# Performance work log

Hardware: AMD Instinct MI355X
Metric: run time of the kernel (lower is better)

The kernel has to match this reference:

```python
import jax, jax.numpy as jnp
import numpy as np

NEG = -1e9  # stand-in for -inf mask fill (avoids NaN, softmax weight ~0)
EPS = 1e-5  # torch LayerNorm default


def layer_norm(x, g, b):
    mu = jnp.mean(x, axis=-1, keepdims=True)
    var = jnp.mean(jnp.square(x - mu), axis=-1, keepdims=True)
    return (x - mu) * jax.lax.rsqrt(var + EPS) * g + b


def _forward(x, context, batch_lengths, max_len,
             Wq1, Wk1, Wv1, Wq2, Wk2, Wv2,
             ln1_g, ln1_b, ln2_g, ln2_b, ln3_g, ln3_b,
             fc1_w, fc1_b, fc2_w, fc2_b):
    B, L, E = x.shape
    H, _, dk = Wq1.shape
    pos = jnp.arange(L)
    valid = pos[None, :] < batch_lengths[:, None]                  # [B,L]
    out_mask = valid[:, :, None].astype(x.dtype)                   # [B,L,1] (outputMask)
    key_bias = jnp.where(valid, 0.0, NEG)[:, None, None, :]        # [B,1,1,L] (attnMask on keys)
    causal_bias = jnp.where(pos[:, None] >= pos[None, :], 0.0, NEG)  # [L,L] decoding mask
    scale = 1.0 / jnp.sqrt(jnp.asarray(dk, x.dtype))

    def mha(qk_src, v_src, Wq, Wk, Wv, causal):
        # Q,K from qk_src, V from v_src (faithful to Head.forward)
        m = out_mask[:, None]                                      # [B,1,L,1]
        Q = jnp.einsum('ble,hed->bhld', qk_src, Wq) * m
        K = jnp.einsum('ble,hed->bhld', qk_src, Wk) * m
        V = jnp.einsum('ble,hed->bhld', v_src, Wv) * m
        e = jnp.einsum('bhid,bhjd->bhij', Q, K) + key_bias
        if causal:
            e = e + causal_bias
        s = jax.nn.softmax(e * scale, axis=-1)
        o = jnp.einsum('bhij,bhjd->bhid', s, V)
        return o.transpose(0, 2, 1, 3).reshape(B, L, E)            # concat heads

    z = mha(x, x, Wq1, Wk1, Wv1, causal=True) * out_mask
    x1 = layer_norm(x + z, ln1_g, ln1_b)
    # cross block: Q,K from context, V from x1 (as in source)
    z = mha(context, x1, Wq2, Wk2, Wv2, causal=False) * out_mask
    x2 = layer_norm(x1 + z, ln2_g, ln2_b)
    h = jax.nn.relu(x2 @ fc1_w + fc1_b) * out_mask
    z = (h @ fc2_w + fc2_b) * out_mask
    return layer_norm(x2 + z, ln3_g, ln3_b)


def setup_inputs() -> dict:
    B, L, E, H = 8, 1024, 1024, 16
    dk = E // H
    key = jax.random.key(0)
    ks = jax.random.split(key, 16)
    w = lambda k, s: jax.random.normal(k, s, jnp.float32) * 0.02
    return {
        'x': jax.random.normal(ks[0], (B, L, E), jnp.float32),
        'context': jax.random.normal(ks[1], (B, L, E), jnp.float32),
        'batch_lengths': jax.random.randint(ks[2], (B,), 1, L + 1),
        'max_len': L,
        'Wq1': w(ks[3], (H, E, dk)), 'Wk1': w(ks[4], (H, E, dk)), 'Wv1': w(ks[5], (H, E, dk)),
        'Wq2': w(ks[6], (H, E, dk)), 'Wk2': w(ks[7], (H, E, dk)), 'Wv2': w(ks[8], (H, E, dk)),
        'ln1_g': jnp.ones((E,), jnp.float32), 'ln1_b': jnp.zeros((E,), jnp.float32),
        'ln2_g': jnp.ones((E,), jnp.float32), 'ln2_b': jnp.zeros((E,), jnp.float32),
        'ln3_g': jnp.ones((E,), jnp.float32), 'ln3_b': jnp.zeros((E,), jnp.float32),
        'fc1_w': w(ks[9], (E, E)), 'fc1_b': jnp.zeros((E,), jnp.float32),
        'fc2_w': w(ks[10], (E, E)), 'fc2_b': jnp.zeros((E,), jnp.float32),
    }


def reference(x, context, batch_lengths, max_len,
              Wq1, Wk1, Wv1, Wq2, Wk2, Wv2,
              ln1_g, ln1_b, ln2_g, ln2_b, ln3_g, ln3_b,
              fc1_w, fc1_b, fc2_w, fc2_b):
    return _forward(x, context, batch_lengths, max_len,
                    Wq1, Wk1, Wv1, Wq2, Wk2, Wv2,
                    ln1_g, ln1_b, ln2_g, ln2_b, ln3_g, ln3_b,
                    fc1_w, fc1_b, fc2_w, fc2_b)
```

## Files before the change

### kernel.cpp

```cpp
#include <hip/hip_runtime.h>


typedef unsigned short u16;
typedef unsigned int u32;
typedef __attribute__((ext_vector_type(8))) short bf16x8;
typedef __attribute__((ext_vector_type(4))) float f32x4;

#define Bv 8
#define Lv 1024
#define Ev 1024
#define Hv 16
#define DKv 64
#define Mv (Bv * Lv)

#if defined(__has_builtin)
# if __has_builtin(__builtin_amdgcn_global_load_lds)
#  define HAS_GLL 1
# endif
#endif
#ifndef HAS_GLL
# define HAS_GLL 0
#endif

#if HAS_GLL
__device__ __forceinline__ void gll16(const u16* g, u16* l) {
    __builtin_amdgcn_global_load_lds(
        (const __attribute__((address_space(1))) void*)(unsigned long long)(g),
        (__attribute__((address_space(3))) void*)(unsigned)(unsigned long long)(l),
        16, 0, 0);
}
#endif

__device__ __forceinline__ u16 f2bf(float f) {
    u32 u = __float_as_uint(f);
    u += 0x7fffu + ((u >> 16) & 1u);
    return (u16)(u >> 16);
}
__device__ __forceinline__ u32 pack2(float a, float b) {
    u32 ua = __float_as_uint(a); ua += 0x7fffu + ((ua >> 16) & 1u);
    u32 ub = __float_as_uint(b); ub += 0x7fffu + ((ub >> 16) & 1u);
    return (ua >> 16) | (ub & 0xffff0000u);
}
__device__ __forceinline__ float bf_lo(u32 u) { return __uint_as_float(u << 16); }
__device__ __forceinline__ float bf_hi(u32 u) { return __uint_as_float(u & 0xffff0000u); }

__global__ __launch_bounds__(256) void prep_k(
    const float* __restrict__ x, const float* __restrict__ ctx,
    const float* __restrict__ wq1, const float* __restrict__ wk1, const float* __restrict__ wv1,
    const float* __restrict__ wq2, const float* __restrict__ wk2, const float* __restrict__ wv2,
    const float* __restrict__ f1, const float* __restrict__ f2,
    u16* __restrict__ xb, u16* __restrict__ cb, u16* __restrict__ WT) {
    const int id = blockIdx.x, t = threadIdx.x;
    if (id < 16384) {
        const float* s = (id < 8192) ? x : ctx;
        u16* d = (id < 8192) ? xb : cb;
        const int i4 = ((id & 8191) * 256 + t) * 4;
        float4 v = *(const float4*)(s + i4);
        uint2 o = {pack2(v.x, v.y), pack2(v.z, v.w)};
        *(uint2*)(d + i4) = o;
        return;
    }
    __shared__ float tl[32][33];
    const int tx = t & 31, ty = t >> 5;
    if (id < 16384 + 6144) {
        const int wi = (id - 16384) >> 10;
        const int tile = (id - 16384) & 1023;
        const float* s = (wi == 0) ? wq1 : (wi == 1) ? wk1 : (wi == 2) ? wv1
                       : (wi == 3) ? wq2 : (wi == 4) ? wk2 : wv2;
        u16* d = WT + (size_t)wi * Ev * Ev;
        const int h = tile >> 6, rem = tile & 63;
        const int d0 = (rem & 1) * 32, e0 = (rem >> 1) * 32;
#pragma unroll
        for (int i = 0; i < 4; i++)
            tl[ty + i * 8][tx] = s[(size_t)h * Ev * DKv + (size_t)(e0 + ty + i * 8) * DKv + d0 + tx];
        __syncthreads();
#pragma unroll
        for (int i = 0; i < 4; i++)
            d[(size_t)(h * DKv + d0 + ty + i * 8) * Ev + e0 + tx] = f2bf(tl[tx][ty + i * 8]);
    } else {
        const int wi = (id - 16384 - 6144) >> 10;
        const int tile = (id - 16384 - 6144) & 1023;
        const float* s = wi ? f2 : f1;
        u16* d = WT + (size_t)(6 + wi) * Ev * Ev;
        const int n0 = (tile & 31) * 32, k0 = (tile >> 5) * 32;
#pragma unroll
        for (int i = 0; i < 4; i++)
            tl[ty + i * 8][tx] = s[(size_t)(k0 + ty + i * 8) * Ev + n0 + tx];
        __syncthreads();
#pragma unroll
        for (int i = 0; i < 4; i++)
            d[(size_t)(n0 + ty + i * 8) * Ev + k0 + tx] = f2bf(tl[tx][ty + i * 8]);
    }
}

template <int BIAS, int RELU, int TRANSW>
__global__ __launch_bounds__(256) void mgemm(const u16* __restrict__ A,
                                             const u16* __restrict__ Wt,
                                             const float* __restrict__ bias,
                                             u16* __restrict__ O0, u16* __restrict__ O1,
                                             u16* __restrict__ O2,
                                             const int* __restrict__ lens) {
    __shared__ u16 Alds[2][16 * 512];
    __shared__ u16 Blds[2][16 * 512];
    const int tid = threadIdx.x;
    const int w = tid >> 6, l = tid & 63;
    const int lc = l & 15, lq = l >> 4;
    const int row0 = blockIdx.y * 128, col0 = blockIdx.x * 128;
    const int which = col0 >> 10, colL = col0 & 1023;
    u16* C = (which == 0) ? O0 : (which == 1 ? O1 : O2);
    const bool tr = (TRANSW == which);

    int len = lens[row0 >> 10];
    len = min(max(len, 0), Lv);
    if ((row0 & (Lv - 1)) >= len) {
        const int rr = tid >> 1, cc = (tid & 1) * 64;
        u16* p = tr ? C + (size_t)(colL + rr) * Mv + row0 + cc
                    : C + (size_t)(row0 + rr) * Ev + colL + cc;
        uint4 z4 = {0u, 0u, 0u, 0u};
#pragma unroll
        for (int i = 0; i < 8; i++) *(uint4*)(p + i * 8) = z4;
        return;
    }

    const int wm4 = (w >> 1) * 4, wn4 = (w & 1) * 4;
    f32x4 acc[4][4];
#pragma unroll
    for (int i = 0; i < 4; i++)
#pragma unroll
        for (int j = 0; j < 4; j++) acc[i][j] = (f32x4){0.f, 0.f, 0.f, 0.f};

    const u16* Ag[4]; const u16* Bg[4];
    int lof[4];
#pragma unroll
    for (int i = 0; i < 4; i++) {
        const int g16 = 2 * w + (i >> 1), k32 = i & 1;
        Ag[i] = A  + (size_t)(row0 + g16 * 16 + lc) * Ev + k32 * 32 + lq * 8;
        Bg[i] = Wt + (size_t)(col0 + g16 * 16 + lc) * Ev + k32 * 32 + lq * 8;
        lof[i] = (g16 * 2 + k32) * 512;
    }

#if HAS_GLL
#pragma unroll
    for (int i = 0; i < 4; i++) { gll16(Ag[i], &Alds[0][lof[i]]); gll16(Bg[i], &Blds[0][lof[i]]); }
#pragma unroll
    for (int i = 0; i < 4; i++) { gll16(Ag[i] + 64, &Alds[1][lof[i]]); gll16(Bg[i] + 64, &Blds[1][lof[i]]); }

    for (int t = 0; t < 16; ++t) {
        const int p = t & 1;
        if (t < 15) asm volatile("s_waitcnt vmcnt(8)" ::: "memory");
        else        asm volatile("s_waitcnt vmcnt(0)" ::: "memory");
        __builtin_amdgcn_s_barrier();
        const u16* Ab = &Alds[p][0];
        const u16* Bb = &Blds[p][0];
#pragma unroll
        for (int km = 0; km < 2; km++) {
            bf16x8 af[4], bfr[4];
#pragma unroll
            for (int mt = 0; mt < 4; mt++)
                af[mt] = *(const bf16x8*)(Ab + ((wm4 + mt) * 2 + km) * 512 + l * 8);
#pragma unroll
            for (int nt = 0; nt < 4; nt++)
                bfr[nt] = *(const bf16x8*)(Bb + ((wn4 + nt) * 2 + km) * 512 + l * 8);
#pragma unroll
            for (int mt = 0; mt < 4; mt++)
#pragma unroll
                for (int nt = 0; nt < 4; nt++)
                    acc[mt][nt] = __builtin_amdgcn_mfma_f32_16x16x32_bf16(
                        af[mt], bfr[nt], acc[mt][nt], 0, 0, 0);
        }
        __builtin_amdgcn_s_barrier();
        if (t < 14) {
            const int koff = (t + 2) * 64;
#pragma unroll
            for (int i = 0; i < 4; i++) {
                gll16(Ag[i] + koff, &Alds[p][lof[i]]);
                gll16(Bg[i] + koff, &Blds[p][lof[i]]);
            }
        }
    }
#else
    for (int t = 0; t < 16; ++t) {
        const int koff = t * 64;
#pragma unroll
        for (int i = 0; i < 4; i++) {
            *(uint4*)(&Alds[0][lof[i] + l * 8]) = *(const uint4*)(Ag[i] + koff);
            *(uint4*)(&Blds[0][lof[i] + l * 8]) = *(const uint4*)(Bg[i] + koff);
        }
        __syncthreads();
#pragma unroll
        for (int km = 0; km < 2; km++) {
            bf16x8 af[4], bfr[4];
#pragma unroll
            for (int mt = 0; mt < 4; mt++)
                af[mt] = *(const bf16x8*)(&Alds[0][((wm4 + mt) * 2 + km) * 512 + l * 8]);
#pragma unroll
            for (int nt = 0; nt < 4; nt++)
                bfr[nt] = *(const bf16x8*)(&Blds[0][((wn4 + nt) * 2 + km) * 512 + l * 8]);
#pragma unroll
            for (int mt = 0; mt < 4; mt++)
#pragma unroll
                for (int nt = 0; nt < 4; nt++)
                    acc[mt][nt] = __builtin_amdgcn_mfma_f32_16x16x32_bf16(
                        af[mt], bfr[nt], acc[mt][nt], 0, 0, 0);
        }
        __syncthreads();
    }
#endif

    float bv[4];
#pragma unroll
    for (int nt = 0; nt < 4; nt++)
        bv[nt] = BIAS ? bias[colL + wn4 * 16 + nt * 16 + lc] : 0.f;

#pragma unroll
    for (int mt = 0; mt < 4; mt++) {
        const int rowb = row0 + wm4 * 16 + mt * 16 + lq * 4;
#pragma unroll
        for (int nt = 0; nt < 4; nt++) {
            const int col = colL + wn4 * 16 + nt * 16 + lc;
            float v[4];
#pragma unroll
            for (int r = 0; r < 4; r++) {
                float xv = acc[mt][nt][r] + bv[nt];
                if (RELU) xv = fmaxf(xv, 0.f);
                v[r] = (((rowb + r) & (Lv - 1)) >= len) ? 0.f : xv;
            }
            if (tr) {
                uint2 o = {pack2(v[0], v[1]), pack2(v[2], v[3])};
                *(uint2*)(C + (size_t)col * Mv + rowb) = o;
            } else {
#pragma unroll
                for (int r = 0; r < 4; r++)
                    C[(size_t)(rowb + r) * Ev + col] = f2bf(v[r]);
            }
        }
    }
}

template <int CAUSAL>
__global__ __launch_bounds__(256) void mattn(u16* __restrict__ QZ,
                                             const u16* __restrict__ K,
                                             const u16* __restrict__ VT,
                                             const int* __restrict__ lens) {
    __shared__ u16 Kt[2][16 * 512];
    __shared__ u16 Vt[2][16 * 512];
    __shared__ u16 Pt[4 * 4 * 512];
    const int b = blockIdx.z, h = blockIdx.y, qb = blockIdx.x;
    const int q0 = qb * 128;
    const int tid = threadIdx.x;
    const int w = tid >> 6, l = tid & 63;
    const int lc = l & 15, lq = l >> 4;
    int len = lens[b];
    len = min(max(len, 0), Lv);

    if (q0 >= len) {
        const int zr = tid >> 1, zc = (tid & 1) * 32;
        uint4 z4 = {0u, 0u, 0u, 0u};
        uint4* p = (uint4*)(QZ + (size_t)(b * Lv + q0 + zr) * Ev + h * DKv + zc);
        p[0] = z4; p[1] = z4; p[2] = z4; p[3] = z4;
        return;
    }

    bf16x8 qf[2][2];
#pragma unroll
    for (int mt = 0; mt < 2; mt++)
#pragma unroll
        for (int k2 = 0; k2 < 2; k2++)
            qf[mt][k2] = *(const bf16x8*)(QZ + (size_t)(b * Lv + q0 + w * 32 + mt * 16 + lc) * Ev +
                                          h * DKv + k2 * 32 + lq * 8);

    f32x4 of[2][4];
#pragma unroll
    for (int mt = 0; mt < 2; mt++)
#pragma unroll
        for (int nd = 0; nd < 4; nd++) of[mt][nd] = (f32x4){0.f, 0.f, 0.f, 0.f};
    float mrow[2][4], lrow[2][4];
#pragma unroll
    for (int mt = 0; mt < 2; mt++)
#pragma unroll
        for (int r = 0; r < 4; r++) { mrow[mt][r] = -1e30f; lrow[mt][r] = 0.f; }

    const u16* Kg[4]; const u16* Vg[4];
    int kof[4], vof[4];
#pragma unroll
    for (int i = 0; i < 4; i++) {
        const int k16 = 2 * w + (i >> 1), d32 = i & 1;
        Kg[i] = K + (size_t)(b * Lv + k16 * 16 + lc) * Ev + h * DKv + d32 * 32 + lq * 8;
        kof[i] = (k16 * 2 + d32) * 512;
        Vg[i] = VT + (size_t)(h * DKv + w * 16 + lc) * Mv + b * Lv + i * 32 + lq * 8;
        vof[i] = (w * 4 + i) * 512;
    }
    u16* Pw = Pt + w * 2048;

    const int jend = CAUSAL ? min(len, q0 + 128) : len;
    const int ntiles = (jend + 127) >> 7;

#if HAS_GLL
#pragma unroll
    for (int i = 0; i < 4; i++) {
        gll16(Kg[i], &Kt[0][kof[i]]);
        gll16(Vg[i], &Vt[0][vof[i]]);
    }
#endif
#if !HAS_GLL
#pragma unroll
    for (int i = 0; i < 4; i++) {
        *(uint4*)(&Kt[0][kof[i] + l * 8]) = *(const uint4*)Kg[i];
        *(uint4*)(&Vt[0][vof[i] + l * 8]) = *(const uint4*)Vg[i];
    }
    __syncthreads();
#endif

    for (int kt = 0; kt < ntiles; kt++) {
        const int p = kt & 1;
        const int koff = kt * 128;
#if HAS_GLL
        if (kt + 1 < ntiles) {
            const int knext = koff + 128;
#pragma unroll
            for (int i = 0; i < 4; i++) {
                gll16(Kg[i] + (size_t)knext * Ev, &Kt[p ^ 1][kof[i]]);
                gll16(Vg[i] + knext, &Vt[p ^ 1][vof[i]]);
            }
            asm volatile("s_waitcnt vmcnt(8)" ::: "memory");
        } else {
            asm volatile("s_waitcnt vmcnt(0)" ::: "memory");
        }
        __builtin_amdgcn_s_barrier();
#else
        if (kt > 0) {
            const int kprev = koff;
#pragma unroll
            for (int i = 0; i < 4; i++) {
                *(uint4*)(&Kt[p][kof[i] + l * 8]) = *(const uint4*)(Kg[i] + (size_t)kprev * Ev);
                *(uint4*)(&Vt[p][vof[i] + l * 8]) = *(const uint4*)(Vg[i] + kprev);
            }
            __syncthreads();
        }
#endif
        const u16* Kb = &Kt[p][0];
        const u16* Vb = &Vt[p][0];

        f32x4 sf[2][8];
#pragma unroll
        for (int nt = 0; nt < 8; nt++) {
            bf16x8 kf0 = *(const bf16x8*)(Kb + (nt * 2 + 0) * 512 + l * 8);
            bf16x8 kf1 = *(const bf16x8*)(Kb + (nt * 2 + 1) * 512 + l * 8);
#pragma unroll
            for (int mt = 0; mt < 2; mt++) {
                f32x4 s = (f32x4){0.f, 0.f, 0.f, 0.f};
                s = __builtin_amdgcn_mfma_f32_16x16x32_bf16(qf[mt][0], kf0, s, 0, 0, 0);
                s = __builtin_amdgcn_mfma_f32_16x16x32_bf16(qf[mt][1], kf1, s, 0, 0, 0);
                sf[mt][nt] = s;
            }
        }

        float alpha[2][4];
#pragma unroll
        for (int mt = 0; mt < 2; mt++) {
            float tmax[4] = {-1e30f, -1e30f, -1e30f, -1e30f};
#pragma unroll
            for (int nt = 0; nt < 8; nt++) {
                const int jj = koff + nt * 16 + lc;
                const bool jv = jj < len;
#pragma unroll
                for (int r = 0; r < 4; r++) {
                    const int iq = q0 + w * 32 + mt * 16 + lq * 4 + r;
                    const bool valid = jv && (!CAUSAL || jj <= iq);
                    float e = valid ? sf[mt][nt][r] * 0.125f : -1e30f;
                    sf[mt][nt][r] = e;
                    tmax[r] = fmaxf(tmax[r], e);
                }
            }
#pragma unroll
            for (int r = 0; r < 4; r++) {
#pragma unroll
                for (int d = 1; d < 16; d <<= 1)
                    tmax[r] = fmaxf(tmax[r], __shfl_xor(tmax[r], d, 64));
            }
            float psum[4];
#pragma unroll
            for (int r = 0; r < 4; r++) {
                const float mn = fmaxf(mrow[mt][r], tmax[r]);
                alpha[mt][r] = __expf(mrow[mt][r] - mn);
                mrow[mt][r] = mn;
                psum[r] = 0.f;
            }
#pragma unroll
            for (int nt = 0; nt < 8; nt++)
#pragma unroll
                for (int r = 0; r < 4; r++) {
                    float p2 = __expf(sf[mt][nt][r] - mrow[mt][r]);
                    sf[mt][nt][r] = p2;
                    psum[r] += p2;
                }
#pragma unroll
            for (int r = 0; r < 4; r++) {
#pragma unroll
                for (int d = 1; d < 16; d <<= 1) psum[r] += __shfl_xor(psum[r], d, 64);
                lrow[mt][r] = lrow[mt][r] * alpha[mt][r] + psum[r];
            }
#pragma unroll
            for (int nd = 0; nd < 4; nd++)
#pragma unroll
                for (int r = 0; r < 4; r++) of[mt][nd][r] *= alpha[mt][r];
        }

#pragma unroll
        for (int mt = 0; mt < 2; mt++) {
#pragma unroll
            for (int nt = 0; nt < 8; nt++)
#pragma unroll
                for (int r = 0; r < 4; r++)
                    Pw[(nt >> 1) * 512 +
                       ((2 * (nt & 1) + (lc >> 3)) * 16 + lq * 4 + r) * 8 + (lc & 7)] =
                        f2bf(sf[mt][nt][r]);
#pragma unroll
            for (int km = 0; km < 4; km++) {
                bf16x8 pa = *(const bf16x8*)(Pw + km * 512 + l * 8);
#pragma unroll
                for (int nd = 0; nd < 4; nd++) {
                    bf16x8 vb = *(const bf16x8*)(Vb + (nd * 4 + km) * 512 + l * 8);
                    of[mt][nd] = __builtin_amdgcn_mfma_f32_16x16x32_bf16(pa, vb, of[mt][nd], 0, 0, 0);
                }
            }
        }
#if HAS_GLL
        __builtin_amdgcn_s_barrier();
#else
        __syncthreads();
#endif
    }

#pragma unroll
    for (int mt = 0; mt < 2; mt++) {
        float inv[4];
#pragma unroll
        for (int r = 0; r < 4; r++) {
            const int iq = q0 + w * 32 + mt * 16 + lq * 4 + r;
            inv[r] = (iq < len && lrow[mt][r] > 0.f) ? (1.f / lrow[mt][r]) : 0.f;
        }
#pragma unroll
        for (int nd = 0; nd < 4; nd++)
#pragma unroll
            for (int r = 0; r < 4; r++)
                QZ[(size_t)(b * Lv + q0 + w * 32 + mt * 16 + lq * 4 + r) * Ev +
                   h * DKv + nd * 16 + lc] = f2bf(of[mt][nd][r] * inv[r]);
    }
}

template <int BASEBF, int OUTF32>
__global__ __launch_bounds__(256) void ln_k(const void* __restrict__ base,
                                            const u16* __restrict__ z,
                                            const float* __restrict__ g,
                                            const float* __restrict__ bta,
                                            void* __restrict__ out) {
    __shared__ float w1[4], w2[4];
    const int row = blockIdx.x, t = threadIdx.x;
    const int w = t >> 6, l = t & 63;
    const int c0 = t * 4;
    float v[4];
    if (BASEBF) {
        uint2 bu = *(const uint2*)((const u16*)base + (size_t)row * Ev + c0);
        v[0] = bf_lo(bu.x); v[1] = bf_hi(bu.x); v[2] = bf_lo(bu.y); v[3] = bf_hi(bu.y);
    } else {
        float4 f = *(const float4*)((const float*)base + (size_t)row * Ev + c0);
        v[0] = f.x; v[1] = f.y; v[2] = f.z; v[3] = f.w;
    }
    uint2 zu = *(const uint2*)(z + (size_t)row * Ev + c0);
    v[0] += bf_lo(zu.x); v[1] += bf_hi(zu.x); v[2] += bf_lo(zu.y); v[3] += bf_hi(zu.y);
    float s1 = v[0] + v[1] + v[2] + v[3];
    float s2 = v[0] * v[0] + v[1] * v[1] + v[2] * v[2] + v[3] * v[3];
#pragma unroll
    for (int d = 1; d < 64; d <<= 1) {
        s1 += __shfl_xor(s1, d, 64);
        s2 += __shfl_xor(s2, d, 64);
    }
    if (l == 0) { w1[w] = s1; w2[w] = s2; }
    __syncthreads();
    s1 = w1[0] + w1[1] + w1[2] + w1[3];
    s2 = w2[0] + w2[1] + w2[2] + w2[3];
    const float mu = s1 * (1.f / Ev);
    const float var = s2 * (1.f / Ev) - mu * mu;
    const float rinv = rsqrtf(fmaxf(var, 0.f) + 1e-5f);
    float4 gv = *(const float4*)(g + c0);
    float4 bv = *(const float4*)(bta + c0);
    float y[4];
    y[0] = (v[0] - mu) * rinv * gv.x + bv.x;
    y[1] = (v[1] - mu) * rinv * gv.y + bv.y;
    y[2] = (v[2] - mu) * rinv * gv.z + bv.z;
    y[3] = (v[3] - mu) * rinv * gv.w + bv.w;
    if (OUTF32) {
        float4 ow = {y[0], y[1], y[2], y[3]};
        *(float4*)((float*)out + (size_t)row * Ev + c0) = ow;
    } else {
        uint2 ow = {pack2(y[0], y[1]), pack2(y[2], y[3])};
        *(uint2*)((u16*)out + (size_t)row * Ev + c0) = ow;
    }
}

extern "C" void kernel_launch(void* const* d_in, const int* in_sizes, int n_in,
                              void* d_out, int out_size, void* d_ws, size_t ws_size,
                              hipStream_t stream) {
    const float* x    = (const float*)d_in[0];
    const float* ctx  = (const float*)d_in[1];
    const int*   lens = (const int*)d_in[2];
    const float* Wq1 = (const float*)d_in[4];
    const float* Wk1 = (const float*)d_in[5];
    const float* Wv1 = (const float*)d_in[6];
    const float* Wq2 = (const float*)d_in[7];
    const float* Wk2 = (const float*)d_in[8];
    const float* Wv2 = (const float*)d_in[9];
    const float* g1 = (const float*)d_in[10], *b1 = (const float*)d_in[11];
    const float* g2 = (const float*)d_in[12], *b2 = (const float*)d_in[13];
    const float* g3 = (const float*)d_in[14], *b3 = (const float*)d_in[15];
    const float* fc1w = (const float*)d_in[16], *fc1b = (const float*)d_in[17];
    const float* fc2w = (const float*)d_in[18], *fc2b = (const float*)d_in[19];

    const size_t WSZ = (size_t)Ev * Ev;
    const size_t MM  = (size_t)Mv * Ev;
    u16* WT = (u16*)d_ws;
    u16* Wtq1 = WT + 0 * WSZ;
    u16* Wtq2 = WT + 3 * WSZ, *Wtv2 = WT + 5 * WSZ;
    u16* Wtf1 = WT + 6 * WSZ, *Wtf2 = WT + 7 * WSZ;
    u16* B1 = WT + 8 * WSZ;
    u16* B2 = B1 + MM;
    u16* B3 = B2 + MM;
    u16* B4 = B3 + MM;
    u16* xb = (u16*)d_out;
    u16* cb = xb + MM;

    dim3 gP(24576), gQKV(24, 64), gQK(16, 64), gG1(8, 64), gA(8, Hv, Bv), gL(Mv);

    prep_k<<<gP, 256, 0, stream>>>(x, ctx, Wq1, Wk1, Wv1, Wq2, Wk2, Wv2, fc1w, fc2w,
                                   xb, cb, WT);

    mgemm<0, 0, 2><<<gQKV, 256, 0, stream>>>(xb, Wtq1, nullptr, B1, B2, B3, lens);
    mattn<1><<<gA, 256, 0, stream>>>(B1, B2, B3, lens);
    ln_k<0, 0><<<gL, 256, 0, stream>>>(x, B1, g1, b1, B2);

    mgemm<0, 0, -1><<<gQK, 256, 0, stream>>>(cb, Wtq2, nullptr, B1, B3, nullptr, lens);
    mgemm<0, 0, 0><<<gG1, 256, 0, stream>>>(B2, Wtv2, nullptr, B4, nullptr, nullptr, lens);
    mattn<0><<<gA, 256, 0, stream>>>(B1, B3, B4, lens);
    ln_k<1, 0><<<gL, 256, 0, stream>>>(B2, B1, g2, b2, B3);

    mgemm<1, 1, -1><<<gG1, 256, 0, stream>>>(B3, Wtf1, fc1b, B1, nullptr, nullptr, lens);
    mgemm<1, 0, -1><<<gG1, 256, 0, stream>>>(B1, Wtf2, fc2b, B2, nullptr, nullptr, lens);
    ln_k<1, 1><<<gL, 256, 0, stream>>>(B3, B2, g3, b3, d_out);
}
```

Measured before the change: 524.9 us.

## Halve GEMM K-tile to cut LDS, raise occupancy, merge cross-attn projections

The GEMM K-step drops from 64 to 32, which halves shared memory per block, and launch_bounds now asks for 4 blocks per CU so more waves can hide load latency. The cross-attention QK and V projections are merged into a single launch through a second A operand, used by the V column block, removing one kernel launch and the tail of a small grid. Compiler memory fences are added around barriers in the GEMM and attention loops to keep LDS accesses ordered. The costs are twice as many barrier and wait cycles per K, fewer MFMAs per sync, and possible register limits from the occupancy hint.

New measurement: 513.2 us. 2.2% less time.

```diff
diff --git a/kernel.cpp b/kernel.cpp
--- a/kernel.cpp
+++ b/kernel.cpp
@@ -30,6 +30,8 @@
         16, 0, 0);
 }
 #endif
+
+#define FENCE() asm volatile("" ::: "memory")
 
 __device__ __forceinline__ u16 f2bf(float f) {
     u32 u = __float_as_uint(f);
@@ -94,14 +96,15 @@
 }
 
 template <int BIAS, int RELU, int TRANSW>
-__global__ __launch_bounds__(256) void mgemm(const u16* __restrict__ A,
-                                             const u16* __restrict__ Wt,
-                                             const float* __restrict__ bias,
-                                             u16* __restrict__ O0, u16* __restrict__ O1,
-                                             u16* __restrict__ O2,
-                                             const int* __restrict__ lens) {
-    __shared__ u16 Alds[2][16 * 512];
-    __shared__ u16 Blds[2][16 * 512];
+__global__ __launch_bounds__(256, 4) void mgemm(const u16* __restrict__ A,
+                                                const u16* __restrict__ Wt,
+                                                const float* __restrict__ bias,
+                                                u16* __restrict__ O0, u16* __restrict__ O1,
+                                                u16* __restrict__ O2,
+                                                const int* __restrict__ lens,
+                                                const u16* __restrict__ A2) {
+    __shared__ u16 Alds[2][8 * 512];
+    __shared__ u16 Blds[2][8 * 512];
     const int tid = threadIdx.x;
     const int w = tid >> 6, l = tid & 63;
     const int lc = l & 15, lq = l >> 4;
@@ -109,6 +112,7 @@
     const int which = col0 >> 10, colL = col0 & 1023;
     u16* C = (which == 0) ? O0 : (which == 1 ? O1 : O2);
     const bool tr = (TRANSW == which);
+    const u16* Aop = (A2 != nullptr && which == 2) ? A2 : A;
 
     int len = lens[row0 >> 10];
     len = min(max(len, 0), Lv);
@@ -129,80 +133,75 @@
 #pragma unroll
         for (int j = 0; j < 4; j++) acc[i][j] = (f32x4){0.f, 0.f, 0.f, 0.f};
 
-    const u16* Ag[4]; const u16* Bg[4];
-    int lof[4];
-#pragma unroll
-    for (int i = 0; i < 4; i++) {
-        const int g16 = 2 * w + (i >> 1), k32 = i & 1;
-        Ag[i] = A  + (size_t)(row0 + g16 * 16 + lc) * Ev + k32 * 32 + lq * 8;
-        Bg[i] = Wt + (size_t)(col0 + g16 * 16 + lc) * Ev + k32 * 32 + lq * 8;
-        lof[i] = (g16 * 2 + k32) * 512;
+    const u16* Ag[2]; const u16* Bg[2];
+    int lof[2];
+#pragma unroll
+    for (int i = 0; i < 2; i++) {
+        const int s = 2 * w + i;
+        Ag[i] = Aop + (size_t)(row0 + s * 16 + lc) * Ev + lq * 8;
+        Bg[i] = Wt  + (size_t)(col0 + s * 16 + lc) * Ev + lq * 8;
+        lof[i] = s * 512;
     }
 
 #if HAS_GLL
 #pragma unroll
-    for (int i = 0; i < 4; i++) { gll16(Ag[i], &Alds[0][lof[i]]); gll16(Bg[i], &Blds[0][lof[i]]); }
-#pragma unroll
-    for (int i = 0; i < 4; i++) { gll16(Ag[i] + 64, &Alds[1][lof[i]]); gll16(Bg[i] + 64, &Blds[1][lof[i]]); }
-
-    for (int t = 0; t < 16; ++t) {
+    for (int i = 0; i < 2; i++) { gll16(Ag[i], &Alds[0][lof[i]]); gll16(Bg[i], &Blds[0][lof[i]]); }
+#pragma unroll
+    for (int i = 0; i < 2; i++) { gll16(Ag[i] + 32, &Alds[1][lof[i]]); gll16(Bg[i] + 32, &Blds[1][lof[i]]); }
+
+    for (int t = 0; t < 32; ++t) {
         const int p = t & 1;
-        if (t < 15) asm volatile("s_waitcnt vmcnt(8)" ::: "memory");
+        if (t < 31) asm volatile("s_waitcnt vmcnt(4)" ::: "memory");
         else        asm volatile("s_waitcnt vmcnt(0)" ::: "memory");
         __builtin_amdgcn_s_barrier();
-        const u16* Ab = &Alds[p][0];
-        const u16* Bb = &Blds[p][0];
-#pragma unroll
-        for (int km = 0; km < 2; km++) {
-            bf16x8 af[4], bfr[4];
-#pragma unroll
-            for (int mt = 0; mt < 4; mt++)
-                af[mt] = *(const bf16x8*)(Ab + ((wm4 + mt) * 2 + km) * 512 + l * 8);
+        FENCE();
+        bf16x8 af[4], bfr[4];
+#pragma unroll
+        for (int mt = 0; mt < 4; mt++)
+            af[mt] = *(const bf16x8*)(&Alds[p][(wm4 + mt) * 512 + l * 8]);
+#pragma unroll
+        for (int nt = 0; nt < 4; nt++)
+            bfr[nt] = *(const bf16x8*)(&Blds[p][(wn4 + nt) * 512 + l * 8]);
+#pragma unroll
+        for (int mt = 0; mt < 4; mt++)
 #pragma unroll
             for (int nt = 0; nt < 4; nt++)
-                bfr[nt] = *(const bf16x8*)(Bb + ((wn4 + nt) * 2 + km) * 512 + l * 8);
-#pragma unroll
-            for (int mt = 0; mt < 4; mt++)
-#pragma unroll
-                for (int nt = 0; nt < 4; nt++)
-                    acc[mt][nt] = __builtin_amdgcn_mfma_f32_16x16x32_bf16(
-                        af[mt], bfr[nt], acc[mt][nt], 0, 0, 0);
-        }
+                acc[mt][nt] = __builtin_amdgcn_mfma_f32_16x16x32_bf16(
+                    af[mt], bfr[nt], acc[mt][nt], 0, 0, 0);
+        FENCE();
         __builtin_amdgcn_s_barrier();
-        if (t < 14) {
-            const int koff = (t + 2) * 64;
-#pragma unroll
-            for (int i = 0; i < 4; i++) {
-                gll16(Ag[i] + koff, &Alds[p][lof[i]]);
-                gll16(Bg[i] + koff, &Blds[p][lof[i]]);
+        FENCE();
+        if (t < 30) {
+            const int ko = (t + 2) * 32;
+#pragma unroll
+            for (int i = 0; i < 2; i++) {
+                gll16(Ag[i] + ko, &Alds[p][lof[i]]);
+                gll16(Bg[i] + ko, &Blds[p][lof[i]]);
             }
         }
     }
 #else
-    for (int t = 0; t < 16; ++t) {
-        const int koff = t * 64;
-#pragma unroll
-        for (int i = 0; i < 4; i++) {
-            *(uint4*)(&Alds[0][lof[i] + l * 8]) = *(const uint4*)(Ag[i] + koff);
-            *(uint4*)(&Blds[0][lof[i] + l * 8]) = *(const uint4*)(Bg[i] + koff);
+    for (int t = 0; t < 32; ++t) {
+        const int ko = t * 32;
+#pragma unroll
+        for (int i = 0; i < 2; i++) {
+            *(uint4*)(&Alds[0][lof[i] + l * 8]) = *(const uint4*)(Ag[i] + ko);
+            *(uint4*)(&Blds[0][lof[i] + l * 8]) = *(const uint4*)(Bg[i] + ko);
         }
         __syncthreads();
-#pragma unroll
-        for (int km = 0; km < 2; km++) {
-            bf16x8 af[4], bfr[4];
-#pragma unroll
-            for (int mt = 0; mt < 4; mt++)
-                af[mt] = *(const bf16x8*)(&Alds[0][((wm4 + mt) * 2 + km) * 512 + l * 8]);
+        bf16x8 af[4], bfr[4];
+#pragma unroll
+        for (int mt = 0; mt < 4; mt++)
+            af[mt] = *(const bf16x8*)(&Alds[0][(wm4 + mt) * 512 + l * 8]);
+#pragma unroll
+        for (int nt = 0; nt < 4; nt++)
+            bfr[nt] = *(const bf16x8*)(&Blds[0][(wn4 + nt) * 512 + l * 8]);
+#pragma unroll
+        for (int mt = 0; mt < 4; mt++)
 #pragma unroll
             for (int nt = 0; nt < 4; nt++)
-                bfr[nt] = *(const bf16x8*)(&Blds[0][((wn4 + nt) * 2 + km) * 512 + l * 8]);
-#pragma unroll
-            for (int mt = 0; mt < 4; mt++)
-#pragma unroll
-                for (int nt = 0; nt < 4; nt++)
-                    acc[mt][nt] = __builtin_amdgcn_mfma_f32_16x16x32_bf16(
-                        af[mt], bfr[nt], acc[mt][nt], 0, 0, 0);
-        }
+                acc[mt][nt] = __builtin_amdgcn_mfma_f32_16x16x32_bf16(
+                    af[mt], bfr[nt], acc[mt][nt], 0, 0, 0);
         __syncthreads();
     }
 #endif
@@ -327,6 +326,7 @@
             asm volatile("s_waitcnt vmcnt(0)" ::: "memory");
         }
         __builtin_amdgcn_s_barrier();
+        FENCE();
 #else
         if (kt > 0) {
             const int kprev = koff;
@@ -426,7 +426,9 @@
             }
         }
 #if HAS_GLL
+        FENCE();
         __builtin_amdgcn_s_barrier();
+        FENCE();
 #else
         __syncthreads();
 #endif
@@ -521,7 +523,7 @@
     const size_t MM  = (size_t)Mv * Ev;
     u16* WT = (u16*)d_ws;
     u16* Wtq1 = WT + 0 * WSZ;
-    u16* Wtq2 = WT + 3 * WSZ, *Wtv2 = WT + 5 * WSZ;
+    u16* Wtq2 = WT + 3 * WSZ;
     u16* Wtf1 = WT + 6 * WSZ, *Wtf2 = WT + 7 * WSZ;
     u16* B1 = WT + 8 * WSZ;
     u16* B2 = B1 + MM;
@@ -530,21 +532,20 @@
     u16* xb = (u16*)d_out;
     u16* cb = xb + MM;
 
-    dim3 gP(24576), gQKV(24, 64), gQK(16, 64), gG1(8, 64), gA(8, Hv, Bv), gL(Mv);
+    dim3 gP(24576), gW(24, 64), gG1(8, 64), gA(8, Hv, Bv), gL(Mv);
 
     prep_k<<<gP, 256, 0, stream>>>(x, ctx, Wq1, Wk1, Wv1, Wq2, Wk2, Wv2, fc1w, fc2w,
                                    xb, cb, WT);
 
-    mgemm<0, 0, 2><<<gQKV, 256, 0, stream>>>(xb, Wtq1, nullptr, B1, B2, B3, lens);
+    mgemm<0, 0, 2><<<gW, 256, 0, stream>>>(xb, Wtq1, nullptr, B1, B2, B3, lens, nullptr);
     mattn<1><<<gA, 256, 0, stream>>>(B1, B2, B3, lens);
     ln_k<0, 0><<<gL, 256, 0, stream>>>(x, B1, g1, b1, B2);
 
-    mgemm<0, 0, -1><<<gQK, 256, 0, stream>>>(cb, Wtq2, nullptr, B1, B3, nullptr, lens);
-    mgemm<0, 0, 0><<<gG1, 256, 0, stream>>>(B2, Wtv2, nullptr, B4, nullptr, nullptr, lens);
+    mgemm<0, 0, 2><<<gW, 256, 0, stream>>>(cb, Wtq2, nullptr, B1, B3, B4, lens, B2);
     mattn<0><<<gA, 256, 0, stream>>>(B1, B3, B4, lens);
     ln_k<1, 0><<<gL, 256, 0, stream>>>(B2, B1, g2, b2, B3);
 
-    mgemm<1, 1, -1><<<gG1, 256, 0, stream>>>(B3, Wtf1, fc1b, B1, nullptr, nullptr, lens);
-    mgemm<1, 0, -1><<<gG1, 256, 0, stream>>>(B1, Wtf2, fc2b, B2, nullptr, nullptr, lens);
+    mgemm<1, 1, -1><<<gG1, 256, 0, stream>>>(B3, Wtf1, fc1b, B1, nullptr, nullptr, lens, nullptr);
+    mgemm<1, 0, -1><<<gG1, 256, 0, stream>>>(B1, Wtf2, fc2b, B2, nullptr, nullptr, lens, nullptr);
     ln_k<1, 1><<<gL, 256, 0, stream>>>(B3, B2, g3, b3, d_out);
 }
```
